# Kernel optimization log

Hardware: AMD Instinct MI355X
Metric: run time of the kernel (lower is better)

Reference implementation:

```python
import jax, jax.numpy as jnp
import numpy as np

# ---- constants matching the original module's globals ----
H = 16          # self.h: number of bit levels; self.n = h per the source
TP = 8          # self.tp: parallel coordinate channels
N_K = 2         # random masks per flipped bit
T = 512         # T_train: tokens per block
N_TRNBR = 128   # neighbor count
K_VOCAB = 128   # sampled vocab count
N_VOCAB = 50257 # full vocab size V for sampled softmax correction
D = 256         # embedding dim
RATIO_COS = 1.0
RATIO_CRO = 0.1
C_CNC = 2 * H * N_K + 1  # candidate locations per token = 65


def setup_inputs() -> dict:
    key = jax.random.key(0)
    ks = jax.random.split(key, 8)
    n = H  # code: self.n = h
    sta_loc = jax.random.randint(ks[0], (T, TP), 1 - n, n, dtype=jnp.int32)
    nei_loc = jax.random.randint(ks[1], (T, N_TRNBR, TP), 1 - n, n, dtype=jnp.int32)
    voc_loc = jax.random.randint(ks[2], (T, K_VOCAB, TP), 1 - n, n, dtype=jnp.int32)
    sta_emb = jax.random.normal(ks[3], (T, D), dtype=jnp.float32)
    nei_emb = jax.random.normal(ks[4], (T, N_TRNBR, D), dtype=jnp.float32)
    voc_emb = jax.random.normal(ks[5], (T, K_VOCAB, D), dtype=jnp.float32)
    # raw random numbers for generate_random_masks: randint(0, self.n)
    rand_masks = jax.random.randint(ks[6], (T, H, N_K, TP), 0, n, dtype=jnp.int32)
    # converge mode: mask is all ones (generate_mask with converge=True)
    mask = jnp.ones((T, N_TRNBR), dtype=bool)
    return {"sta_loc": sta_loc, "nei_loc": nei_loc, "voc_loc": voc_loc,
            "sta_emb": sta_emb, "nei_emb": nei_emb, "voc_emb": voc_emb,
            "rand_masks": rand_masks, "mask": mask}


def _cos_similarity(c1, c2):
    # sign product: (+1 if >=0 else -1) for each operand
    sg = ((2 * (c1 >= 0).astype(jnp.int32) - 1) *
          (2 * (c2 >= 0).astype(jnp.int32) - 1)).astype(jnp.float32)
    x = ((jnp.abs(c1) ^ jnp.abs(c2)) + 1).astype(jnp.float32)
    # torch.frexp exponent of v>=1 equals floor(log2(v)) + 1
    expo = jnp.floor(jnp.log2(x)) + 1.0
    return sg * (1.0 - expo / H)


def _connection(sta_loc, rand_masks):
    bits = jnp.arange(H, dtype=jnp.int32)
    flip_masks = (1 << bits)                          # [H]
    flipped = sta_loc[:, None, :] ^ flip_masks[None, :, None]  # [T,H,TP]
    # note operator precedence in source: rn & (2**i - 1)
    rm = rand_masks & (flip_masks - 1)[None, :, None, None]    # [T,H,N_K,TP]
    res = (flipped[:, :, None, :] ^ rm).reshape(sta_loc.shape[0], H * N_K, TP)
    return jnp.concatenate([res, sta_loc[:, None, :], -res], axis=1)  # [T,C,TP]


def _normalize(x):
    return x / jnp.maximum(jnp.linalg.norm(x, axis=-1, keepdims=True), 1e-12)


def reference(sta_loc, nei_loc, voc_loc, sta_emb, nei_emb, voc_emb, rand_masks, mask):
    cnc_loc = _connection(sta_loc, rand_masks)          # [T, C, TP]
    lth = mask.sum(axis=1).astype(jnp.float32) + 1e-12  # [T]

    # euclidean-space cosine targets: [T, N_trnbr]
    eu_cos_val = jnp.einsum('td,tnd->tn', _normalize(sta_emb), _normalize(nei_emb))
    # use_eu_norm == True branch: ||sta|| * ||voc|| -> [T, K_vocab]
    eu_cro_nrm = (jnp.linalg.norm(sta_emb, axis=-1, keepdims=True) *
                  jnp.linalg.norm(voc_emb, axis=-1))

    pos_loc = jnp.concatenate([nei_loc, voc_loc], axis=1)           # [T, P, TP]
    cos_sta_pos = _cos_similarity(sta_loc[:, None, :], pos_loc)     # [T, P, TP]
    cos_sta_pos_sum = cos_sta_pos.sum(axis=-1)                      # [T, P]
    cos_cnc_pos = _cos_similarity(cnc_loc[:, None, :, :], pos_loc[:, :, None, :])  # [T,P,C,TP]
    ct_val = (cos_sta_pos_sum[:, :, None, None]
              - cos_sta_pos[:, :, None, :] + cos_cnc_pos) / TP      # [T,P,C,TP]

    # cosine-matching loss over neighbors
    eu = eu_cos_val[:, :, None, None]                               # [T,N,1,1]
    loss_cos = ((ct_val[:, :N_TRNBR] - eu) ** 2 * jnp.abs(eu)
                * mask[:, :, None, None].astype(jnp.float32))
    loss_cos = loss_cos.sum(axis=1) / lth[:, None, None]            # [T, C, TP]

    # sampled softmax CE (uniform proposal), positive class at vocab index 0
    z = ct_val[:, N_TRNBR:] * eu_cro_nrm[:, :, None, None]          # [T, K, C, TP]
    corr = jnp.where(jnp.arange(K_VOCAB) == 0, 0.0,
                     jnp.log(N_VOCAB / K_VOCAB)).astype(jnp.float32)
    zc = z + corr[None, :, None, None]
    loss_cro = jax.scipy.special.logsumexp(zc, axis=1) - zc[:, 0]   # [T, C, TP]

    loss_tot = RATIO_COS * loss_cos + RATIO_CRO * loss_cro

    # get_best_loc with cur_portion=1.0, cur_tp=tp -> pure argmin selection
    idx = jnp.argmin(loss_tot, axis=1)                              # [T, TP]
    gather = lambda a: jnp.take_along_axis(a, idx[:, None, :], axis=1)[:, 0]
    selected_locs = gather(cnc_loc)                                 # [T, TP]
    real_loss_cos = gather(loss_cos).mean(axis=-1)                  # [T]
    real_loss_cro = gather(loss_cro).mean(axis=-1)
    real_loss_tot = gather(loss_tot).mean(axis=-1)
    return selected_locs, real_loss_cos, real_loss_cro, real_loss_tot
```

## Files before the change

### kernel.cpp

```cpp
#include <hip/hip_runtime.h>
#include <math.h>

#define T_DIM 512
#define TP 8
#define NC 65
#define NJ 128
#define BLOCK 576
#define LOG2E 1.4426950408889634f
#define LN2   0.6931471805599453f
#define CORR_L2 8.617045f

__device__ __forceinline__ float i2f(int x) { return __int_as_float(x); }
__device__ __forceinline__ int   f2i(float x) { return __float_as_int(x); }

__global__ __launch_bounds__(BLOCK) void cg_main(
    const int* __restrict__ sta_loc,
    const int* __restrict__ nei_loc,
    const int* __restrict__ voc_loc,
    const float* __restrict__ sta_emb,
    const float* __restrict__ nei_emb,
    const float* __restrict__ voc_emb,
    const int* __restrict__ rand_masks,
    float* __restrict__ wcos,
    float* __restrict__ wcro)
{
    const int t = blockIdx.x;
    const int side = blockIdx.y;
    const int tid = threadIdx.x;

    __shared__ int4  s_pc4[NJ * TP];
    __shared__ float s_cspT[TP * 132];
    __shared__ float s_css[NJ];
    __shared__ float s_w[NJ];
    __shared__ float s_dot[NJ], s_nn[NJ];
    __shared__ float s_Mpart[9 * 8];
    __shared__ float s_ss;
    __shared__ int   s_sta[TP];
    __shared__ int   s_rand[256];

    if (tid < TP) s_sta[tid] = sta_loc[t * TP + tid];
    if (tid < 256) s_rand[tid] = rand_masks[t * 256 + tid];

    if (tid < 512) {
        const float* emb = side ? voc_emb : nei_emb;
        const int g = tid >> 2, sub = tid & 3;
        const float4* ep = (const float4*)(emb + ((size_t)t * NJ + g) * 256);
        const float4* sp = (const float4*)(sta_emb + (size_t)t * 256);
        float dd = 0.f, nn = 0.f, ss = 0.f;
        #pragma unroll
        for (int i = 0; i < 16; ++i) {
            const int i4 = sub + 4 * i;
            const float4 b = ep[i4];
            nn += b.x * b.x + b.y * b.y + b.z * b.z + b.w * b.w;
            if (side == 0) {
                const float4 a = sp[i4];
                dd += a.x * b.x + a.y * b.y + a.z * b.z + a.w * b.w;
            }
            if (g == 0) {
                const float4 a = sp[i4];
                ss += a.x * a.x + a.y * a.y + a.z * a.z + a.w * a.w;
            }
        }
        nn += __shfl_xor(nn, 1); nn += __shfl_xor(nn, 2);
        if (side == 0) { dd += __shfl_xor(dd, 1); dd += __shfl_xor(dd, 2); }
        if (g == 0)    { ss += __shfl_xor(ss, 1); ss += __shfl_xor(ss, 2); }
        if (sub == 0) {
            s_nn[g] = nn;
            if (side == 0) s_dot[g] = dd;
            if (g == 0) s_ss = ss;
        }
    }
    __syncthreads();

    {
        const int* loc = side ? voc_loc : nei_loc;
        for (int item = tid; item < NJ * TP; item += BLOCK) {
            const int pl = loc[t * (NJ * TP) + item];
            const int qa = pl < 0 ? -pl : pl;
            const int qsgn = pl & 0x80000000;
            const int sta = s_sta[item & 7];
            const int sa = sta < 0 ? -sta : sta;
            const int x = sa ^ qa;
            const float u0 = fmaf((float)__clz(x + 1), 0.0625f, -1.0f);
            const float csp = i2f(f2i(u0) ^ ((sta ^ pl) & 0x80000000));
            ((int2*)&s_pc4[item])[0] = make_int2(qa, qsgn);
            s_cspT[(item & 7) * 132 + (item >> 3)] = csp;
        }
    }
    __syncthreads();

    if (tid < NJ) {
        float cs = 0.f;
        #pragma unroll
        for (int p = 0; p < TP; ++p) cs += s_cspT[p * 132 + tid];
        s_css[tid] = cs;
        const float ns = sqrtf(s_ss);
        const float nn = s_nn[tid];
        if (side == 0)
            s_w[tid] = s_dot[tid] / (fmaxf(sqrtf(nn), 1e-12f) * fmaxf(ns, 1e-12f));
        else
            s_w[tid] = ns * sqrtf(nn) * (0.125f * LOG2E);
    }
    __syncthreads();

    {
        float mloc = -INFINITY;
        for (int item = tid; item < NJ * TP; item += BLOCK) {
            const int j = item >> 3, p = item & 7;
            const float csp = s_cspT[p * 132 + j];
            const float b = s_css[j] - csp;
            const float w = s_w[j];
            float z2, w2;
            if (side == 0) { z2 = fmaf(b, 0.125f, -w); w2 = fabsf(w); }
            else {
                z2 = fmaf(b, w, j ? CORR_L2 : 0.0f);
                w2 = w;
                mloc = fmaxf(mloc, z2 + w);
            }
            ((int2*)&s_pc4[item])[1] = make_int2(f2i(z2), f2i(w2));
        }
        if (side) {
            mloc = fmaxf(mloc, __shfl_xor(mloc, 8));
            mloc = fmaxf(mloc, __shfl_xor(mloc, 16));
            mloc = fmaxf(mloc, __shfl_xor(mloc, 32));
            const int lane = tid & 63;
            if (lane < 8) s_Mpart[(tid >> 6) * 8 + lane] = mloc;
        }
    }
    __syncthreads();

    if (tid < NC * TP) {
        const int c = tid >> 3, p = tid & 7;
        const int sta = s_sta[p];
        int v;
        if (c == 32) v = sta;
        else {
            const int cc = (c < 32) ? c : (c - 33);
            const int h = cc >> 1;
            const int r = (sta ^ (1 << h)) ^ (s_rand[cc * TP + p] & ((1 << h) - 1));
            v = (c < 32) ? r : -r;
        }
        const int va = v < 0 ? -v : v;
        const int vs = v & 0x80000000;
        const int4* pc = s_pc4 + p;

        if (side == 0) {
            float lc0 = 0.f, lc1 = 0.f;
            #pragma unroll 2
            for (int j = 0; j < NJ; j += 2) {
                const int4 a = pc[j * 8];
                const int4 b = pc[(j + 1) * 8];
                {
                    const int x = va ^ a.x;
                    const float u8 = fmaf((float)__clz(x + 1), 0.0078125f, -0.125f);
                    const float d = i2f(f2i(u8) ^ (vs ^ a.y)) + i2f(a.z);
                    lc0 = fmaf(d * d, i2f(a.w), lc0);
                }
                {
                    const int x = va ^ b.x;
                    const float u8 = fmaf((float)__clz(x + 1), 0.0078125f, -0.125f);
                    const float d = i2f(f2i(u8) ^ (vs ^ b.y)) + i2f(b.z);
                    lc1 = fmaf(d * d, i2f(b.w), lc1);
                }
            }
            wcos[t * (NC * TP) + tid] = (lc0 + lc1) * 0.0078125f;
        } else {
            float M = s_Mpart[p];
            #pragma unroll
            for (int w = 1; w < 9; ++w) M = fmaxf(M, s_Mpart[w * 8 + p]);
            float z0;
            {
                const int4 a = pc[0];
                const int x = va ^ a.x;
                const float u0 = fmaf((float)__clz(x + 1), 0.0625f, -1.0f);
                const float u = i2f(f2i(u0) ^ (vs ^ a.y));
                z0 = fmaf(u, i2f(a.w), i2f(a.z)) - M;
            }
            float s0 = __builtin_amdgcn_exp2f(z0), s1;
            {
                const int4 a = pc[8];
                const int x = va ^ a.x;
                const float u0 = fmaf((float)__clz(x + 1), 0.0625f, -1.0f);
                const float u = i2f(f2i(u0) ^ (vs ^ a.y));
                s1 = __builtin_amdgcn_exp2f(fmaf(u, i2f(a.w), i2f(a.z)) - M);
            }
            #pragma unroll 2
            for (int k = 2; k < NJ; k += 2) {
                const int4 a = pc[k * 8];
                const int4 b = pc[(k + 1) * 8];
                {
                    const int x = va ^ a.x;
                    const float u0 = fmaf((float)__clz(x + 1), 0.0625f, -1.0f);
                    const float u = i2f(f2i(u0) ^ (vs ^ a.y));
                    s0 += __builtin_amdgcn_exp2f(fmaf(u, i2f(a.w), i2f(a.z)) - M);
                }
                {
                    const int x = va ^ b.x;
                    const float u0 = fmaf((float)__clz(x + 1), 0.0625f, -1.0f);
                    const float u = i2f(f2i(u0) ^ (vs ^ b.y));
                    s1 += __builtin_amdgcn_exp2f(fmaf(u, i2f(b.w), i2f(b.z)) - M);
                }
            }
            const float S = fmaxf(s0 + s1, 1e-38f);
            wcro[t * (NC * TP) + tid] = (__builtin_amdgcn_logf(S) - z0) * LN2;
        }
    }
}

__global__ __launch_bounds__(128) void cg_fin(
    const int* __restrict__ sta_loc, const int* __restrict__ rand_masks,
    const float* __restrict__ wcos, const float* __restrict__ wcro,
    float* __restrict__ out)
{
    const int t = blockIdx.x, tid = threadIdx.x;
    __shared__ float sc[NC * TP], sr[NC * TP];
    for (int i = tid; i < NC * TP; i += 128) {
        sc[i] = wcos[t * (NC * TP) + i];
        sr[i] = wcro[t * (NC * TP) + i];
    }
    __syncthreads();
    float vc = 0.f, vr = 0.f, vt = 0.f;
    if (tid < TP) {
        float best = INFINITY, blc = 0.f, blr = 0.f;
        int bc = 0;
        for (int c = 0; c < NC; ++c) {
            const float lc = sc[c * TP + tid];
            const float lr = sr[c * TP + tid];
            const float lt = fmaf(0.1f, lr, lc);
            if (lt < best) { best = lt; bc = c; blc = lc; blr = lr; }
        }
        const int sta = sta_loc[t * TP + tid];
        int v;
        if (bc == 32) v = sta;
        else {
            const int cc = (bc < 32) ? bc : (bc - 33);
            const int h = cc >> 1;
            const int r = (sta ^ (1 << h)) ^ (rand_masks[t * 256 + cc * TP + tid] & ((1 << h) - 1));
            v = (bc < 32) ? r : -r;
        }
        out[t * TP + tid] = (float)v;
        vc = blc; vr = blr; vt = best;
    }
    vc += __shfl_xor(vc, 1); vc += __shfl_xor(vc, 2); vc += __shfl_xor(vc, 4);
    vr += __shfl_xor(vr, 1); vr += __shfl_xor(vr, 2); vr += __shfl_xor(vr, 4);
    vt += __shfl_xor(vt, 1); vt += __shfl_xor(vt, 2); vt += __shfl_xor(vt, 4);
    if (tid == 0) {
        out[T_DIM * TP + t] = vc * 0.125f;
        out[T_DIM * TP + T_DIM + t] = vr * 0.125f;
        out[T_DIM * TP + 2 * T_DIM + t] = vt * 0.125f;
    }
}

extern "C" void kernel_launch(void* const* d_in, const int* in_sizes, int n_in,
                              void* d_out, int out_size, void* d_ws, size_t ws_size,
                              hipStream_t stream) {
    const int* sta_loc = (const int*)d_in[0];
    const int* nei_loc = (const int*)d_in[1];
    const int* voc_loc = (const int*)d_in[2];
    const float* sta_emb = (const float*)d_in[3];
    const float* nei_emb = (const float*)d_in[4];
    const float* voc_emb = (const float*)d_in[5];
    const int* rand_masks = (const int*)d_in[6];
    float* out = (float*)d_out;

    float* wcos = (float*)d_ws;
    float* wcro = wcos + (size_t)T_DIM * NC * TP;

    cg_main<<<dim3(T_DIM, 2), BLOCK, 0, stream>>>(
        sta_loc, nei_loc, voc_loc, sta_emb, nei_emb, voc_emb, rand_masks, wcos, wcro);
    cg_fin<<<T_DIM, 128, 0, stream>>>(sta_loc, rand_masks, wcos, wcro, out);
}
```

Measured before the change: 210.1 us.

## Fuse both loss sides and argmin finalize into a single kernel per token

```diff
diff --git a/kernel.cpp b/kernel.cpp
--- a/kernel.cpp
+++ b/kernel.cpp
@@ -5,7 +5,7 @@
 #define TP 8
 #define NC 65
 #define NJ 128
-#define BLOCK 576
+#define BLOCK 512
 #define LOG2E 1.4426950408889634f
 #define LN2   0.6931471805599453f
 #define CORR_L2 8.617045f
@@ -13,7 +13,75 @@
 __device__ __forceinline__ float i2f(int x) { return __int_as_float(x); }
 __device__ __forceinline__ int   f2i(float x) { return __float_as_int(x); }
 
-__global__ __launch_bounds__(BLOCK) void cg_main(
+__device__ __forceinline__ float body_cos(int va, int vs, const int4* pc) {
+    float lc0 = 0.f, lc1 = 0.f;
+    #pragma unroll 2
+    for (int j = 0; j < NJ; j += 2) {
+        const int4 a = pc[j * 8];
+        const int4 b = pc[(j + 1) * 8];
+        {
+            const int x = va ^ a.x;
+            const float u8 = fmaf((float)__clz(x + 1), 0.0078125f, -0.125f);
+            const float d = i2f(f2i(u8) ^ (vs ^ a.y)) + i2f(a.z);
+            lc0 = fmaf(d * d, i2f(a.w), lc0);
+        }
+        {
+            const int x = va ^ b.x;
+            const float u8 = fmaf((float)__clz(x + 1), 0.0078125f, -0.125f);
+            const float d = i2f(f2i(u8) ^ (vs ^ b.y)) + i2f(b.z);
+            lc1 = fmaf(d * d, i2f(b.w), lc1);
+        }
+    }
+    return (lc0 + lc1) * 0.0078125f;
+}
+
+__device__ __forceinline__ float body_cro(int va, int vs, const int4* pc, float M) {
+    float z0;
+    {
+        const int4 a = pc[0];
+        const int x = va ^ a.x;
+        const float u0 = fmaf((float)__clz(x + 1), 0.0625f, -1.0f);
+        const float u = i2f(f2i(u0) ^ (vs ^ a.y));
+        z0 = fmaf(u, i2f(a.w), i2f(a.z)) - M;
+    }
+    float s0 = __builtin_amdgcn_exp2f(z0), s1;
+    {
+        const int4 a = pc[8];
+        const int x = va ^ a.x;
+        const float u0 = fmaf((float)__clz(x + 1), 0.0625f, -1.0f);
+        const float u = i2f(f2i(u0) ^ (vs ^ a.y));
+        s1 = __builtin_amdgcn_exp2f(fmaf(u, i2f(a.w), i2f(a.z)) - M);
+    }
+    #pragma unroll 2
+    for (int k = 2; k < NJ; k += 2) {
+        const int4 a = pc[k * 8];
+        const int4 b = pc[(k + 1) * 8];
+        {
+            const int x = va ^ a.x;
+            const float u0 = fmaf((float)__clz(x + 1), 0.0625f, -1.0f);
+            const float u = i2f(f2i(u0) ^ (vs ^ a.y));
+            s0 += __builtin_amdgcn_exp2f(fmaf(u, i2f(a.w), i2f(a.z)) - M);
+        }
+        {
+            const int x = va ^ b.x;
+            const float u0 = fmaf((float)__clz(x + 1), 0.0625f, -1.0f);
+            const float u = i2f(f2i(u0) ^ (vs ^ b.y));
+            s1 += __builtin_amdgcn_exp2f(fmaf(u, i2f(b.w), i2f(b.z)) - M);
+        }
+    }
+    const float S = fmaxf(s0 + s1, 1e-38f);
+    return (__builtin_amdgcn_logf(S) - z0) * LN2;
+}
+
+__device__ __forceinline__ int cand_v(int c, int sta, const int* s_rand, int p) {
+    if (c == 32) return sta;
+    const int cc = (c < 32) ? c : (c - 33);
+    const int h = cc >> 1;
+    const int r = (sta ^ (1 << h)) ^ (s_rand[cc * TP + p] & ((1 << h) - 1));
+    return (c < 32) ? r : -r;
+}
+
+__global__ __launch_bounds__(BLOCK, 4) void cg_fused(
     const int* __restrict__ sta_loc,
     const int* __restrict__ nei_loc,
     const int* __restrict__ voc_loc,
@@ -21,19 +89,19 @@
     const float* __restrict__ nei_emb,
     const float* __restrict__ voc_emb,
     const int* __restrict__ rand_masks,
-    float* __restrict__ wcos,
-    float* __restrict__ wcro)
+    float* __restrict__ out)
 {
     const int t = blockIdx.x;
-    const int side = blockIdx.y;
     const int tid = threadIdx.x;
 
-    __shared__ int4  s_pc4[NJ * TP];
-    __shared__ float s_cspT[TP * 132];
-    __shared__ float s_css[NJ];
-    __shared__ float s_w[NJ];
-    __shared__ float s_dot[NJ], s_nn[NJ];
-    __shared__ float s_Mpart[9 * 8];
+    __shared__ int4  s_pc4[2][NJ * TP];
+    __shared__ float s_cspT[2][TP * 132];
+    __shared__ float s_css[2][NJ];
+    __shared__ float s_w[2][NJ];
+    __shared__ float s_dot[NJ];
+    __shared__ float s_nn[2][NJ];
+    __shared__ float s_lcos[NC * TP], s_lcro[NC * TP];
+    __shared__ float s_Mpart[8 * 8];
     __shared__ float s_ss;
     __shared__ int   s_sta[TP];
     __shared__ int   s_rand[256];
@@ -41,75 +109,76 @@
     if (tid < TP) s_sta[tid] = sta_loc[t * TP + tid];
     if (tid < 256) s_rand[tid] = rand_masks[t * 256 + tid];
 
-    if (tid < 512) {
-        const float* emb = side ? voc_emb : nei_emb;
-        const int g = tid >> 2, sub = tid & 3;
-        const float4* ep = (const float4*)(emb + ((size_t)t * NJ + g) * 256);
-        const float4* sp = (const float4*)(sta_emb + (size_t)t * 256);
+    {
+        const int idx = tid >> 1, sub = tid & 1;
+        const int side_r = idx & 1, row = idx >> 1;
+        const float* emb = side_r ? voc_emb : nei_emb;
+        const float4* ep = (const float4*)(emb + ((size_t)t * NJ + row) * 256) + sub * 32;
+        const float4* sp = (const float4*)(sta_emb + (size_t)t * 256) + sub * 32;
         float dd = 0.f, nn = 0.f, ss = 0.f;
-        #pragma unroll
-        for (int i = 0; i < 16; ++i) {
-            const int i4 = sub + 4 * i;
-            const float4 b = ep[i4];
+        #pragma unroll 4
+        for (int i = 0; i < 32; ++i) {
+            const float4 b = ep[i];
             nn += b.x * b.x + b.y * b.y + b.z * b.z + b.w * b.w;
-            if (side == 0) {
-                const float4 a = sp[i4];
+            if (side_r == 0) {
+                const float4 a = sp[i];
                 dd += a.x * b.x + a.y * b.y + a.z * b.z + a.w * b.w;
+                if (row == 0) ss += a.x * a.x + a.y * a.y + a.z * a.z + a.w * a.w;
             }
-            if (g == 0) {
-                const float4 a = sp[i4];
-                ss += a.x * a.x + a.y * a.y + a.z * a.z + a.w * a.w;
-            }
-        }
-        nn += __shfl_xor(nn, 1); nn += __shfl_xor(nn, 2);
-        if (side == 0) { dd += __shfl_xor(dd, 1); dd += __shfl_xor(dd, 2); }
-        if (g == 0)    { ss += __shfl_xor(ss, 1); ss += __shfl_xor(ss, 2); }
+        }
+        nn += __shfl_xor(nn, 1);
+        if (side_r == 0) { dd += __shfl_xor(dd, 1); ss += __shfl_xor(ss, 1); }
         if (sub == 0) {
-            s_nn[g] = nn;
-            if (side == 0) s_dot[g] = dd;
-            if (g == 0) s_ss = ss;
-        }
-    }
-    __syncthreads();
-
-    {
-        const int* loc = side ? voc_loc : nei_loc;
-        for (int item = tid; item < NJ * TP; item += BLOCK) {
-            const int pl = loc[t * (NJ * TP) + item];
+            s_nn[side_r][row] = nn;
+            if (side_r == 0) { s_dot[row] = dd; if (row == 0) s_ss = ss; }
+        }
+    }
+
+    {
+        #pragma unroll
+        for (int k = 0; k < 4; ++k) {
+            const int item = tid + k * 512;
+            const int side = item >> 10, idx = item & 1023;
+            const int* loc = side ? voc_loc : nei_loc;
+            const int pl = loc[t * (NJ * TP) + idx];
             const int qa = pl < 0 ? -pl : pl;
             const int qsgn = pl & 0x80000000;
-            const int sta = s_sta[item & 7];
+            const int sta = s_sta[idx & 7];
             const int sa = sta < 0 ? -sta : sta;
             const int x = sa ^ qa;
             const float u0 = fmaf((float)__clz(x + 1), 0.0625f, -1.0f);
             const float csp = i2f(f2i(u0) ^ ((sta ^ pl) & 0x80000000));
-            ((int2*)&s_pc4[item])[0] = make_int2(qa, qsgn);
-            s_cspT[(item & 7) * 132 + (item >> 3)] = csp;
-        }
-    }
-    __syncthreads();
-
-    if (tid < NJ) {
+            ((int2*)&s_pc4[side][idx])[0] = make_int2(qa, qsgn);
+            s_cspT[side][(idx & 7) * 132 + (idx >> 3)] = csp;
+        }
+    }
+    __syncthreads();
+
+    if (tid < 256) {
+        const int j = tid >> 1, side = tid & 1;
         float cs = 0.f;
         #pragma unroll
-        for (int p = 0; p < TP; ++p) cs += s_cspT[p * 132 + tid];
-        s_css[tid] = cs;
+        for (int p = 0; p < TP; ++p) cs += s_cspT[side][p * 132 + j];
+        s_css[side][j] = cs;
         const float ns = sqrtf(s_ss);
-        const float nn = s_nn[tid];
+        const float nn = s_nn[side][j];
         if (side == 0)
-            s_w[tid] = s_dot[tid] / (fmaxf(sqrtf(nn), 1e-12f) * fmaxf(ns, 1e-12f));
+            s_w[0][j] = s_dot[j] / (fmaxf(sqrtf(nn), 1e-12f) * fmaxf(ns, 1e-12f));
         else
-            s_w[tid] = ns * sqrtf(nn) * (0.125f * LOG2E);
+            s_w[1][j] = ns * sqrtf(nn) * (0.125f * LOG2E);
     }
     __syncthreads();
 
     {
         float mloc = -INFINITY;
-        for (int item = tid; item < NJ * TP; item += BLOCK) {
-            const int j = item >> 3, p = item & 7;
-            const float csp = s_cspT[p * 132 + j];
-            const float b = s_css[j] - csp;
-            const float w = s_w[j];
+        #pragma unroll
+        for (int k = 0; k < 4; ++k) {
+            const int item = tid + k * 512;
+            const int side = item >> 10, idx = item & 1023;
+            const int j = idx >> 3, p = idx & 7;
+            const float csp = s_cspT[side][p * 132 + j];
+            const float b = s_css[side][j] - csp;
+            const float w = s_w[side][j];
             float z2, w2;
             if (side == 0) { z2 = fmaf(b, 0.125f, -w); w2 = fabsf(w); }
             else {
@@ -117,137 +186,63 @@
                 w2 = w;
                 mloc = fmaxf(mloc, z2 + w);
             }
-            ((int2*)&s_pc4[item])[1] = make_int2(f2i(z2), f2i(w2));
-        }
-        if (side) {
-            mloc = fmaxf(mloc, __shfl_xor(mloc, 8));
-            mloc = fmaxf(mloc, __shfl_xor(mloc, 16));
-            mloc = fmaxf(mloc, __shfl_xor(mloc, 32));
-            const int lane = tid & 63;
-            if (lane < 8) s_Mpart[(tid >> 6) * 8 + lane] = mloc;
-        }
-    }
-    __syncthreads();
-
-    if (tid < NC * TP) {
-        const int c = tid >> 3, p = tid & 7;
-        const int sta = s_sta[p];
-        int v;
-        if (c == 32) v = sta;
-        else {
-            const int cc = (c < 32) ? c : (c - 33);
-            const int h = cc >> 1;
-            const int r = (sta ^ (1 << h)) ^ (s_rand[cc * TP + p] & ((1 << h) - 1));
-            v = (c < 32) ? r : -r;
-        }
-        const int va = v < 0 ? -v : v;
-        const int vs = v & 0x80000000;
-        const int4* pc = s_pc4 + p;
-
-        if (side == 0) {
-            float lc0 = 0.f, lc1 = 0.f;
-            #pragma unroll 2
-            for (int j = 0; j < NJ; j += 2) {
-                const int4 a = pc[j * 8];
-                const int4 b = pc[(j + 1) * 8];
-                {
-                    const int x = va ^ a.x;
-                    const float u8 = fmaf((float)__clz(x + 1), 0.0078125f, -0.125f);
-                    const float d = i2f(f2i(u8) ^ (vs ^ a.y)) + i2f(a.z);
-                    lc0 = fmaf(d * d, i2f(a.w), lc0);
-                }
-                {
-                    const int x = va ^ b.x;
-                    const float u8 = fmaf((float)__clz(x + 1), 0.0078125f, -0.125f);
-                    const float d = i2f(f2i(u8) ^ (vs ^ b.y)) + i2f(b.z);
-                    lc1 = fmaf(d * d, i2f(b.w), lc1);
+            ((int2*)&s_pc4[side][idx])[1] = make_int2(f2i(z2), f2i(w2));
+        }
+        mloc = fmaxf(mloc, __shfl_xor(mloc, 8));
+        mloc = fmaxf(mloc, __shfl_xor(mloc, 16));
+        mloc = fmaxf(mloc, __shfl_xor(mloc, 32));
+        const int lane = tid & 63;
+        if (lane < 8) s_Mpart[(tid >> 6) * 8 + lane] = mloc;
+    }
+    __syncthreads();
+
+    {
+        #pragma unroll
+        for (int pass = 0; pass < 3; ++pass) {
+            const int u = tid + pass * 512;
+            if (u < 2 * NC * TP) {
+                const int side = (u >= NC * TP);
+                const int w = u - side * (NC * TP);
+                const int c = w >> 3, p = w & 7;
+                const int v = cand_v(c, s_sta[p], s_rand, p);
+                const int va = v < 0 ? -v : v;
+                const int vs = v & 0x80000000;
+                if (side == 0) {
+                    s_lcos[w] = body_cos(va, vs, s_pc4[0] + p);
+                } else {
+                    float M = s_Mpart[p];
+                    #pragma unroll
+                    for (int wv = 1; wv < 8; ++wv) M = fmaxf(M, s_Mpart[wv * 8 + p]);
+                    s_lcro[w] = body_cro(va, vs, s_pc4[1] + p, M);
                 }
             }
-            wcos[t * (NC * TP) + tid] = (lc0 + lc1) * 0.0078125f;
-        } else {
-            float M = s_Mpart[p];
-            #pragma unroll
-            for (int w = 1; w < 9; ++w) M = fmaxf(M, s_Mpart[w * 8 + p]);
-            float z0;
-            {
-                const int4 a = pc[0];
-                const int x = va ^ a.x;
-                const float u0 = fmaf((float)__clz(x + 1), 0.0625f, -1.0f);
-                const float u = i2f(f2i(u0) ^ (vs ^ a.y));
-                z0 = fmaf(u, i2f(a.w), i2f(a.z)) - M;
-            }
-            float s0 = __builtin_amdgcn_exp2f(z0), s1;
-            {
-                const int4 a = pc[8];
-                const int x = va ^ a.x;
-                const float u0 = fmaf((float)__clz(x + 1), 0.0625f, -1.0f);
-                const float u = i2f(f2i(u0) ^ (vs ^ a.y));
-                s1 = __builtin_amdgcn_exp2f(fmaf(u, i2f(a.w), i2f(a.z)) - M);
-            }
-            #pragma unroll 2
-            for (int k = 2; k < NJ; k += 2) {
-                const int4 a = pc[k * 8];
-                const int4 b = pc[(k + 1) * 8];
-                {
-                    const int x = va ^ a.x;
-                    const float u0 = fmaf((float)__clz(x + 1), 0.0625f, -1.0f);
-                    const float u = i2f(f2i(u0) ^ (vs ^ a.y));
-                    s0 += __builtin_amdgcn_exp2f(fmaf(u, i2f(a.w), i2f(a.z)) - M);
-                }
-                {
-                    const int x = va ^ b.x;
-                    const float u0 = fmaf((float)__clz(x + 1), 0.0625f, -1.0f);
-                    const float u = i2f(f2i(u0) ^ (vs ^ b.y));
-                    s1 += __builtin_amdgcn_exp2f(fmaf(u, i2f(b.w), i2f(b.z)) - M);
-                }
-            }
-            const float S = fmaxf(s0 + s1, 1e-38f);
-            wcro[t * (NC * TP) + tid] = (__builtin_amdgcn_logf(S) - z0) * LN2;
-        }
-    }
-}
-
-__global__ __launch_bounds__(128) void cg_fin(
-    const int* __restrict__ sta_loc, const int* __restrict__ rand_masks,
-    const float* __restrict__ wcos, const float* __restrict__ wcro,
-    float* __restrict__ out)
-{
-    const int t = blockIdx.x, tid = threadIdx.x;
-    __shared__ float sc[NC * TP], sr[NC * TP];
-    for (int i = tid; i < NC * TP; i += 128) {
-        sc[i] = wcos[t * (NC * TP) + i];
-        sr[i] = wcro[t * (NC * TP) + i];
-    }
-    __syncthreads();
+        }
+    }
+    __syncthreads();
+
     float vc = 0.f, vr = 0.f, vt = 0.f;
     if (tid < TP) {
+        const int p = tid;
         float best = INFINITY, blc = 0.f, blr = 0.f;
         int bc = 0;
         for (int c = 0; c < NC; ++c) {
-            const float lc = sc[c * TP + tid];
-            const float lr = sr[c * TP + tid];
+            const float lc = s_lcos[c * TP + p];
+            const float lr = s_lcro[c * TP + p];
             const float lt = fmaf(0.1f, lr, lc);
             if (lt < best) { best = lt; bc = c; blc = lc; blr = lr; }
         }
-        const int sta = sta_loc[t * TP + tid];
-        int v;
-        if (bc == 32) v = sta;
-        else {
-            const int cc = (bc < 32) ? bc : (bc - 33);
-            const int h = cc >> 1;
-            const int r = (sta ^ (1 << h)) ^ (rand_masks[t * 256 + cc * TP + tid] & ((1 << h) - 1));
-            v = (bc < 32) ? r : -r;
-        }
-        out[t * TP + tid] = (float)v;
+        out[t * TP + p] = (float)cand_v(bc, s_sta[p], s_rand, p);
         vc = blc; vr = blr; vt = best;
     }
-    vc += __shfl_xor(vc, 1); vc += __shfl_xor(vc, 2); vc += __shfl_xor(vc, 4);
-    vr += __shfl_xor(vr, 1); vr += __shfl_xor(vr, 2); vr += __shfl_xor(vr, 4);
-    vt += __shfl_xor(vt, 1); vt += __shfl_xor(vt, 2); vt += __shfl_xor(vt, 4);
-    if (tid == 0) {
-        out[T_DIM * TP + t] = vc * 0.125f;
-        out[T_DIM * TP + T_DIM + t] = vr * 0.125f;
-        out[T_DIM * TP + 2 * T_DIM + t] = vt * 0.125f;
+    if (tid < 64) {
+        vc += __shfl_xor(vc, 1); vc += __shfl_xor(vc, 2); vc += __shfl_xor(vc, 4);
+        vr += __shfl_xor(vr, 1); vr += __shfl_xor(vr, 2); vr += __shfl_xor(vr, 4);
+        vt += __shfl_xor(vt, 1); vt += __shfl_xor(vt, 2); vt += __shfl_xor(vt, 4);
+        if (tid == 0) {
+            out[T_DIM * TP + t] = vc * 0.125f;
+            out[T_DIM * TP + T_DIM + t] = vr * 0.125f;
+            out[T_DIM * TP + 2 * T_DIM + t] = vt * 0.125f;
+        }
     }
 }
 
@@ -263,10 +258,6 @@
     const int* rand_masks = (const int*)d_in[6];
     float* out = (float*)d_out;
 
-    float* wcos = (float*)d_ws;
-    float* wcro = wcos + (size_t)T_DIM * NC * TP;
-
-    cg_main<<<dim3(T_DIM, 2), BLOCK, 0, stream>>>(
-        sta_loc, nei_loc, voc_loc, sta_emb, nei_emb, voc_emb, rand_masks, wcos, wcro);
-    cg_fin<<<T_DIM, 128, 0, stream>>>(sta_loc, rand_masks, wcos, wcro, out);
-}
+    cg_fused<<<T_DIM, BLOCK, 0, stream>>>(
+        sta_loc, nei_loc, voc_loc, sta_emb, nei_emb, voc_emb, rand_masks, out);
+}
```

New measurement: 223.9 us. 6.6% more time.
